# Kernel tuning notes

Measured on AMD Instinct MI355X. Metric: run time of the kernel, lower is better.

The kernel has to match this reference:

```python
import jax, jax.numpy as jnp
import numpy as np

SEQ, BATCH = 256, 8
N_NODES = SEQ * BATCH
VOCAB, D_MODEL, H, D_K, D_FF, N_LAYERS, MAX_POS = 259, 256, 8, 32, 1024, 2, 128


def setup_inputs() -> dict:
    key = jax.random.key(0)
    ks = jax.random.split(key, 16)
    # structured causal edge list per sequence (dst attends to src <= dst, incl. self)
    tri_dst, tri_src = np.tril_indices(SEQ)
    offs = (np.arange(BATCH) * SEQ)[:, None]
    edge_src = jnp.asarray((tri_src[None, :] + offs).ravel(), dtype=jnp.int64)
    edge_dst = jnp.asarray((tri_dst[None, :] + offs).ravel(), dtype=jnp.int64)
    positions = jnp.tile(jnp.arange(SEQ, dtype=jnp.int64), BATCH)
    tokens = jax.random.randint(ks[0], (N_NODES,), 0, VOCAB, dtype=jnp.int64)
    s = 0.02
    p = lambda k, shp: jax.random.normal(k, shp, dtype=jnp.float32) * s
    return {
        "tokens": tokens, "positions": positions,
        "edge_src": edge_src, "edge_dst": edge_dst,
        "coord_emb": p(ks[1], (3, D_MODEL)),
        "pos_emb": p(ks[2], (MAX_POS, D_MODEL)),
        "value_emb": p(ks[3], (VOCAB, D_MODEL)),
        "ln1_scale": jnp.ones((N_LAYERS, D_MODEL)), "ln1_bias": jnp.zeros((N_LAYERS, D_MODEL)),
        "Wqkv": p(ks[4], (N_LAYERS, D_MODEL, 3 * D_MODEL)),
        "Wo": p(ks[5], (N_LAYERS, D_MODEL, D_MODEL)),
        "ln2_scale": jnp.ones((N_LAYERS, D_MODEL)), "ln2_bias": jnp.zeros((N_LAYERS, D_MODEL)),
        "W1": p(ks[6], (N_LAYERS, D_MODEL, D_FF)), "b1": jnp.zeros((N_LAYERS, D_FF)),
        "W2": p(ks[7], (N_LAYERS, D_FF, D_MODEL)), "b2": jnp.zeros((N_LAYERS, D_MODEL)),
        "lnf_scale": jnp.ones((D_MODEL,)), "lnf_bias": jnp.zeros((D_MODEL,)),
        "Wg": p(ks[8], (D_MODEL, VOCAB)), "bg": jnp.zeros((VOCAB,)),
    }


def _ln(x, scale, bias, eps=1e-5):
    mu = jnp.mean(x, axis=-1, keepdims=True)
    var = jnp.var(x, axis=-1, keepdims=True)
    return (x - mu) * jax.lax.rsqrt(var + eps) * scale + bias


def _graph_attention(x, src, dst, Wqkv, Wo, ln_s, ln_b):
    n = x.shape[0]
    xn = _ln(x, ln_s, ln_b)
    qkv = (xn @ Wqkv).reshape(n, 3, H, D_K)
    q, k, v = qkv[:, 0], qkv[:, 1], qkv[:, 2]  # [n, H, D_K] each
    # u_dot_v('k','q','score') per edge, scaled
    score = jnp.einsum("ehd,ehd->eh", k[src], q[dst]) / jnp.sqrt(jnp.float32(D_K))
    # edge_softmax over incoming edges of each dst node
    smax = jax.ops.segment_max(score, dst, num_segments=n)      # [n, H]
    ex = jnp.exp(score - smax[dst])                              # [E, H]
    denom = jax.ops.segment_sum(ex, dst, num_segments=n)        # [n, H]
    alpha = ex / denom[dst]
    # u_mul_e('v','softmax_score') + sum reduce -> z on dst nodes
    z = jax.ops.segment_sum(alpha[:, :, None] * v[src], dst, num_segments=n)  # [n, H, D_K]
    return x + z.reshape(n, D_MODEL) @ Wo


def reference(tokens, positions, edge_src, edge_dst, coord_emb, pos_emb, value_emb,
              ln1_scale, ln1_bias, Wqkv, Wo, ln2_scale, ln2_bias, W1, b1, W2, b2,
              lnf_scale, lnf_bias, Wg, bg):
    x = coord_emb[positions % 3] + pos_emb[positions // 3] + value_emb[tokens]
    for i in range(Wqkv.shape[0]):
        x = _graph_attention(x, edge_src, edge_dst, Wqkv[i], Wo[i], ln1_scale[i], ln1_bias[i])
        h = _ln(x, ln2_scale[i], ln2_bias[i])
        x = x + jax.nn.relu(h @ W1[i] + b1[i]) @ W2[i] + b2[i]
    out = _ln(x, lnf_scale, lnf_bias) @ Wg + bg
    return jax.nn.log_softmax(out, axis=-1)
```

## Files before the change

### kernel.cpp

```cpp
#include <hip/hip_runtime.h>
#include <hip/hip_bf16.h>

typedef __hip_bfloat16 bf16;
typedef unsigned short ushort_t;
typedef unsigned int uint_t;
typedef __attribute__((ext_vector_type(8))) short short8;
typedef __attribute__((ext_vector_type(4))) float floatx4;

#define D_MODEL 256
#define SEQ     256
#define BATCH   8
#define NN      2048
#define NHEAD   8
#define DK      32
#define DFF     1024
#define VOCAB   259
#define NLAYER  2

#define WQKVT_OFF 0
#define WOT_OFF   393216
#define W1T_OFF   524288
#define W2T_OFF   1048576
#define WGT_OFF   1572864
#define WT_TOTAL  1639168
#define LNP_TOTAL 2560
#define BP_TOTAL  2819

template<bool BF>
__device__ __forceinline__ float ldw(const void* p, int i) {
    if (BF) return __bfloat162float(((const bf16*)p)[i]);
    return ((const float*)p)[i];
}
template<bool BF>
__device__ __forceinline__ ushort_t ldb(const void* p, size_t i) {
    if (BF) return ((const ushort_t*)p)[i];
    bf16 h = __float2bfloat16(((const float*)p)[i]);
    ushort_t u; __builtin_memcpy(&u, &h, 2); return u;
}
template<bool I64>
__device__ __forceinline__ int ldi(const void* p, int i) {
    if (I64) return (int)(((const long long*)p)[i]);
    return ((const int*)p)[i];
}
__device__ __forceinline__ ushort_t f2bs(float f) {
    bf16 h = __float2bfloat16(f);
    ushort_t u; __builtin_memcpy(&u, &h, 2); return u;
}
__device__ __forceinline__ float bs2f(uint_t u16) {
    return __uint_as_float(u16 << 16);
}
__device__ __forceinline__ float wred_sum(float v) {
    #pragma unroll
    for (int m = 32; m > 0; m >>= 1) v += __shfl_xor(v, m, 64);
    return v;
}
__device__ __forceinline__ float wred_max(float v) {
    #pragma unroll
    for (int m = 32; m > 0; m >>= 1) v = fmaxf(v, __shfl_xor(v, m, 64));
    return v;
}
__device__ __forceinline__ bool detBF(const void* ln1s) {
    return *(const uint_t*)ln1s == 0x3F803F80u;
}
__device__ __forceinline__ bool detI64(const void* pos) {
    const int* p32 = (const int*)pos;
    return p32[1] == 0 && p32[2] == 1;
}

template<bool BF>
__device__ void ttile(const void* src, size_t srcOff, int K, int N, int tk, int tn,
                      ushort_t* dst, ushort_t (*tile)[68]) {
    int t = threadIdx.x;
    #pragma unroll
    for (int pass = 0; pass < 16; ++pass) {
        int e = pass * 256 + t;
        int kl = e >> 6, nl = e & 63;
        int n = tn * 64 + nl;
        tile[kl][nl] = (n < N) ? ldb<BF>(src, srcOff + (size_t)(tk*64 + kl) * N + n)
                               : (ushort_t)0;
    }
    __syncthreads();
    #pragma unroll
    for (int pass = 0; pass < 16; ++pass) {
        int e = pass * 256 + t;
        int nl = e >> 6, kl = e & 63;
        int n = tn * 64 + nl;
        if (n < N) dst[(size_t)n * K + tk*64 + kl] = tile[kl][nl];
    }
}

template<bool BF, bool I64>
__device__ void embedln16(const void* tok, const void* pos,
        const void* ce, const void* pe, const void* ve,
        const void* ln1s, const void* ln1b, int rowBase,
        float* x, ushort_t* xn) {
    int lane = threadIdx.x & 63, wave = threadIdx.x >> 6;
    #pragma unroll
    for (int i = 0; i < 4; ++i) {
        int n = rowBase + wave * 4 + i;
        int p  = ldi<I64>(pos, n);
        int tk = ldi<I64>(tok, n);
        int c0 = lane * 4;
        float v[4];
        #pragma unroll
        for (int j = 0; j < 4; ++j)
            v[j] = ldw<BF>(ce, (p % 3) * 256 + c0 + j)
                 + ldw<BF>(pe, (p / 3) * 256 + c0 + j)
                 + ldw<BF>(ve, tk * 256 + c0 + j);
        float s  = wred_sum(v[0] + v[1] + v[2] + v[3]);
        float s2 = wred_sum(v[0]*v[0] + v[1]*v[1] + v[2]*v[2] + v[3]*v[3]);
        float mu = s * (1.f/256.f);
        float var = s2 * (1.f/256.f) - mu * mu;
        float rstd = rsqrtf(var + 1e-5f);
        *reinterpret_cast<float4*>(&x[(size_t)n*256 + c0]) =
            make_float4(v[0], v[1], v[2], v[3]);
        ushort4 o;
        o.x = f2bs((v[0]-mu)*rstd*ldw<BF>(ln1s, c0+0) + ldw<BF>(ln1b, c0+0));
        o.y = f2bs((v[1]-mu)*rstd*ldw<BF>(ln1s, c0+1) + ldw<BF>(ln1b, c0+1));
        o.z = f2bs((v[2]-mu)*rstd*ldw<BF>(ln1s, c0+2) + ldw<BF>(ln1b, c0+2));
        o.w = f2bs((v[3]-mu)*rstd*ldw<BF>(ln1s, c0+3) + ldw<BF>(ln1b, c0+3));
        *reinterpret_cast<ushort4*>(&xn[(size_t)n*256 + c0]) = o;
    }
}

template<bool BF, bool I64>
__device__ void prep_body(const void* tok, const void* pos,
        const void* ce, const void* pe, const void* ve,
        const void* Wqkv, const void* Wo, const void* W1, const void* W2, const void* Wg,
        const void* ln1s, const void* ln1b, const void* ln2s, const void* ln2b,
        const void* lnfs, const void* lnfb,
        const void* b1, const void* b2, const void* bg,
        ushort_t* WT, float* lnP, float* bP, float* x, ushort_t* xn,
        ushort_t (*tile)[68]) {
    int blk = blockIdx.x;
    if (blk < 404) {
        const void* src; int K, N, tk, tn; size_t dstOff, srcOff;
        if (blk < 96)       { int L = blk/48, lo = blk%48; src=Wqkv; K=256; N=768;
                              srcOff=(size_t)L*196608; dstOff=WQKVT_OFF+(size_t)L*196608;
                              tk=lo/12; tn=lo%12; }
        else if (blk < 128) { int b2=blk-96, L=b2/16, lo=b2%16; src=Wo; K=256; N=256;
                              srcOff=(size_t)L*65536; dstOff=WOT_OFF+(size_t)L*65536;
                              tk=lo/4; tn=lo%4; }
        else if (blk < 256) { int b2=blk-128, L=b2/64, lo=b2%64; src=W1; K=256; N=1024;
                              srcOff=(size_t)L*262144; dstOff=W1T_OFF+(size_t)L*262144;
                              tk=lo/16; tn=lo%16; }
        else if (blk < 384) { int b2=blk-256, L=b2/64, lo=b2%64; src=W2; K=1024; N=256;
                              srcOff=(size_t)L*262144; dstOff=W2T_OFF+(size_t)L*262144;
                              tk=lo/4; tn=lo%4; }
        else                { int lo=blk-384; src=Wg; K=256; N=259;
                              srcOff=0; dstOff=WGT_OFF; tk=lo/5; tn=lo%5; }
        ttile<BF>(src, srcOff, K, N, tk, tn, WT + dstOff, tile);
    } else if (blk < 426) {
        int gid = (blk - 404) * 256 + threadIdx.x;
        if (gid < LNP_TOTAL) {
            float v;
            if      (gid < 512)  v = ldw<BF>(ln1s, gid);
            else if (gid < 1024) v = ldw<BF>(ln1b, gid - 512);
            else if (gid < 1536) v = ldw<BF>(ln2s, gid - 1024);
            else if (gid < 2048) v = ldw<BF>(ln2b, gid - 1536);
            else if (gid < 2304) v = ldw<BF>(lnfs, gid - 2048);
            else                 v = ldw<BF>(lnfb, gid - 2304);
            lnP[gid] = v;
        } else if (gid < LNP_TOTAL + BP_TOTAL) {
            int g = gid - LNP_TOTAL;
            float v;
            if      (g < 2048) v = ldw<BF>(b1, g);
            else if (g < 2560) v = ldw<BF>(b2, g - 2048);
            else               v = ldw<BF>(bg, g - 2560);
            bP[g] = v;
        }
    } else {
        embedln16<BF, I64>(tok, pos, ce, pe, ve, ln1s, ln1b, (blk - 426) * 16, x, xn);
    }
}

__global__ void __launch_bounds__(256) prep_k(const void* tok, const void* pos,
        const void* ce, const void* pe, const void* ve,
        const void* Wqkv, const void* Wo, const void* W1, const void* W2, const void* Wg,
        const void* ln1s, const void* ln1b, const void* ln2s, const void* ln2b,
        const void* lnfs, const void* lnfb,
        const void* b1, const void* b2, const void* bg,
        ushort_t* WT, float* lnP, float* bP, float* x, ushort_t* xn) {
    __shared__ ushort_t tile[64][68];
    bool BF = detBF(ln1s), I64 = detI64(pos);
    if (BF) { if (I64) prep_body<true,true >(tok,pos,ce,pe,ve,Wqkv,Wo,W1,W2,Wg,ln1s,ln1b,ln2s,ln2b,lnfs,lnfb,b1,b2,bg,WT,lnP,bP,x,xn,tile);
              else     prep_body<true,false>(tok,pos,ce,pe,ve,Wqkv,Wo,W1,W2,Wg,ln1s,ln1b,ln2s,ln2b,lnfs,lnfb,b1,b2,bg,WT,lnP,bP,x,xn,tile); }
    else    { if (I64) prep_body<false,true >(tok,pos,ce,pe,ve,Wqkv,Wo,W1,W2,Wg,ln1s,ln1b,ln2s,ln2b,lnfs,lnfb,b1,b2,bg,WT,lnP,bP,x,xn,tile);
              else     prep_body<false,false>(tok,pos,ce,pe,ve,Wqkv,Wo,W1,W2,Wg,ln1s,ln1b,ln2s,ln2b,lnfs,lnfb,b1,b2,bg,WT,lnP,bP,x,xn,tile); }
}

union AttnSH {
    struct {
        ushort_t Ks[SEQ][40];
        ushort_t Qs[64][40];
    } a;
    ushort_t Ps[64][264];
};
__global__ void __launch_bounds__(256) attn_k(const ushort_t* __restrict__ qkvB,
                                              ushort_t* __restrict__ zB) {
    __shared__ AttnSH u;
    __shared__ ushort_t Vt[32][264];
    int t = threadIdx.x;
    int lane = t & 63, wave = t >> 6;
    int quad = lane >> 4, l16 = lane & 15;
    int tile = blockIdx.x & 3, bh = blockIdx.x >> 2;
    int b = bh >> 3, h = bh & 7;
    int base = b * SEQ;
    int dstBase = tile * 64;
    int tileEnd = (tile + 1) * 64;

    int nV = tileEnd * 4;
    for (int i = t; i < nV; i += 256) {
        int src = i >> 2, g = i & 3;
        const ushort_t* rp = qkvB + (size_t)(base + src) * 768 + h * 32 + g * 8;
        uint4 kv = *reinterpret_cast<const uint4*>(rp + 256);
        *reinterpret_cast<uint4*>(&u.a.Ks[src][g * 8]) = kv;
        uint4 vv = *reinterpret_cast<const uint4*>(rp + 512);
        const ushort_t* vs = (const ushort_t*)&vv;
        #pragma unroll
        for (int j = 0; j < 8; ++j) Vt[g * 8 + j][src] = vs[j];
    }
    {
        int r = t >> 2, g = t & 3;
        uint4 qv = *reinterpret_cast<const uint4*>(
            qkvB + (size_t)(base + dstBase + r) * 768 + h * 32 + g * 8);
        *reinterpret_cast<uint4*>(&u.a.Qs[r][g * 8]) = qv;
    }
    __syncthreads();

    const float scale = 0.17677669529663687f;
    int stLim = tile * 4 + wave;
    int stCnt = stLim + 1;
    short8 qf = *reinterpret_cast<const short8*>(&u.a.Qs[wave * 16 + l16][quad * 8]);
    floatx4 accs[16];
    #pragma unroll
    for (int st = 0; st < 16; ++st) {
        if (st <= stLim) {
            short8 kf = *reinterpret_cast<const short8*>(&u.a.Ks[st * 16 + l16][quad * 8]);
            accs[st] = __builtin_amdgcn_mfma_f32_16x16x32_bf16(qf, kf, (floatx4){0.f,0.f,0.f,0.f}, 0, 0, 0);
        }
    }
    float mrow[4] = {-3e38f, -3e38f, -3e38f, -3e38f};
    #pragma unroll
    for (int st = 0; st < 16; ++st) {
        if (st <= stLim) {
            int srcg = st * 16 + l16;
            #pragma unroll
            for (int r = 0; r < 4; ++r) {
                int dstg = dstBase + wave * 16 + quad * 4 + r;
                float sv = (srcg <= dstg) ? accs[st][r] * scale : -3e38f;
                accs[st][r] = sv;
                mrow[r] = fmaxf(mrow[r], sv);
            }
        }
    }
    #pragma unroll
    for (int mk = 1; mk < 16; mk <<= 1)
        #pragma unroll
        for (int r = 0; r < 4; ++r) mrow[r] = fmaxf(mrow[r], __shfl_xor(mrow[r], mk, 64));
    float lrow[4] = {0.f, 0.f, 0.f, 0.f};
    #pragma unroll
    for (int st = 0; st < 16; ++st) {
        if (st <= stLim) {
            #pragma unroll
            for (int r = 0; r < 4; ++r) {
                float p = __expf(accs[st][r] - mrow[r]);
                accs[st][r] = p;
                lrow[r] += p;
            }
        }
    }
    #pragma unroll
    for (int mk = 1; mk < 16; mk <<= 1)
        #pragma unroll
        for (int r = 0; r < 4; ++r) lrow[r] += __shfl_xor(lrow[r], mk, 64);
    __syncthreads();

    #pragma unroll
    for (int st = 0; st < 16; ++st) {
        if (st <= stLim) {
            #pragma unroll
            for (int r = 0; r < 4; ++r)
                u.Ps[wave * 16 + quad * 4 + r][st * 16 + l16] = f2bs(accs[st][r]);
        }
    }
    if (stCnt & 1) {
        #pragma unroll
        for (int r = 0; r < 4; ++r)
            u.Ps[wave * 16 + quad * 4 + r][stCnt * 16 + l16] = 0;
    }
    __syncthreads();

    int ktCnt = (stCnt + 1) >> 1;
    floatx4 acco[2];
    acco[0] = (floatx4){0.f,0.f,0.f,0.f};
    acco[1] = (floatx4){0.f,0.f,0.f,0.f};
    #pragma unroll
    for (int kt = 0; kt < 8; ++kt) {
        if (kt < ktCnt) {
            short8 pf = *reinterpret_cast<const short8*>(&u.Ps[wave * 16 + l16][kt * 32 + quad * 8]);
            #pragma unroll
            for (int dn = 0; dn < 2; ++dn) {
                short8 vf = *reinterpret_cast<const short8*>(&Vt[dn * 16 + l16][kt * 32 + quad * 8]);
                acco[dn] = __builtin_amdgcn_mfma_f32_16x16x32_bf16(pf, vf, acco[dn], 0, 0, 0);
            }
        }
    }
    #pragma unroll
    for (int dn = 0; dn < 2; ++dn)
        #pragma unroll
        for (int r = 0; r < 4; ++r)
            zB[(size_t)(base + dstBase + wave * 16 + quad * 4 + r) * 256
               + h * 32 + dn * 16 + l16] = f2bs(acco[dn][r] / lrow[r]);
}

__global__ void __launch_bounds__(256) gemm_k(const ushort_t* __restrict__ A, int K,
        const ushort_t* __restrict__ BT, const float* __restrict__ bias,
        ushort_t* __restrict__ C, int ldc, int relu) {
    int t = threadIdx.x;
    int lane = t & 63, wave = t >> 6;
    int quad = lane >> 4, l16 = lane & 15;
    int wm = (wave >> 1) * 32, wn = (wave & 1) * 32;
    int rowBase = blockIdx.x * 64, colBase = blockIdx.y * 64;
    floatx4 acc[2][2];
    #pragma unroll
    for (int a = 0; a < 2; ++a)
        #pragma unroll
        for (int b = 0; b < 2; ++b) acc[a][b] = (floatx4){0.f,0.f,0.f,0.f};
    const ushort_t* a0 = A + (size_t)(rowBase + wm + l16) * K + quad * 8;
    const ushort_t* a1 = a0 + (size_t)16 * K;
    const ushort_t* b0 = BT + (size_t)(colBase + wn + l16) * K + quad * 8;
    const ushort_t* b1 = b0 + (size_t)16 * K;
    #pragma unroll 8
    for (int k0 = 0; k0 < K; k0 += 32) {
        short8 af0 = *reinterpret_cast<const short8*>(a0 + k0);
        short8 af1 = *reinterpret_cast<const short8*>(a1 + k0);
        short8 bf0 = *reinterpret_cast<const short8*>(b0 + k0);
        short8 bf1 = *reinterpret_cast<const short8*>(b1 + k0);
        acc[0][0] = __builtin_amdgcn_mfma_f32_16x16x32_bf16(af0, bf0, acc[0][0], 0,0,0);
        acc[0][1] = __builtin_amdgcn_mfma_f32_16x16x32_bf16(af0, bf1, acc[0][1], 0,0,0);
        acc[1][0] = __builtin_amdgcn_mfma_f32_16x16x32_bf16(af1, bf0, acc[1][0], 0,0,0);
        acc[1][1] = __builtin_amdgcn_mfma_f32_16x16x32_bf16(af1, bf1, acc[1][1], 0,0,0);
    }
    #pragma unroll
    for (int nt = 0; nt < 2; ++nt) {
        int col = colBase + wn + nt*16 + l16;
        float bb = bias ? bias[col] : 0.f;
        #pragma unroll
        for (int mt = 0; mt < 2; ++mt)
            #pragma unroll
            for (int r = 0; r < 4; ++r) {
                int row = rowBase + wm + mt*16 + quad*4 + r;
                float v = acc[mt][nt][r] + bb;
                if (relu) v = fmaxf(v, 0.f);
                C[(size_t)row * ldc + col] = f2bs(v);
            }
    }
}

__global__ void __launch_bounds__(256) gemmresln_k(const ushort_t* __restrict__ A, int K,
        const ushort_t* __restrict__ BT, const float* __restrict__ bias,
        float* __restrict__ x, const float* __restrict__ ls, const float* __restrict__ lb,
        ushort_t* __restrict__ xnG,
        const void* __restrict__ ln1sRaw, const ushort_t* __restrict__ WgT,
        const float* __restrict__ bgP, void* __restrict__ outp, int doLogits) {
    __shared__ float sparts[4][16][256];
    __shared__ ushort_t xnS[16][264];
    float (*Lg)[273] = reinterpret_cast<float (*)[273]>(&sparts[1][0][0]);
    int t = threadIdx.x;
    int lane = t & 63, wave = t >> 6;
    int quad = lane >> 4, l16 = lane & 15;
    int rowBase = blockIdx.x * 16;
    int Kq = K >> 2;
    int wk0 = wave * Kq;

    {
        floatx4 acc[16];
        #pragma unroll
        for (int nt = 0; nt < 16; ++nt) acc[nt] = (floatx4){0.f,0.f,0.f,0.f};
        const ushort_t* a0 = A + (size_t)(rowBase + l16) * K + wk0 + quad * 8;
        for (int k0 = 0; k0 < Kq; k0 += 32) {
            short8 af = *reinterpret_cast<const short8*>(a0 + k0);
            #pragma unroll
            for (int nt = 0; nt < 16; ++nt) {
                short8 bv = *reinterpret_cast<const short8*>(
                    BT + (size_t)(nt*16 + l16) * K + wk0 + k0 + quad * 8);
                acc[nt] = __builtin_amdgcn_mfma_f32_16x16x32_bf16(af, bv, acc[nt], 0,0,0);
            }
        }
        #pragma unroll
        for (int nt = 0; nt < 16; ++nt)
            #pragma unroll
            for (int r = 0; r < 4; ++r)
                sparts[wave][quad*4 + r][nt*16 + l16] = acc[nt][r];
    }
    __syncthreads();
    {
        float* flat0 = &sparts[0][0][0];
        #pragma unroll
        for (int i = 0; i < 16; ++i) {
            int idx = i * 256 + t;
            int row = idx >> 8, col = idx & 255;
            float v = flat0[idx] + (&sparts[1][0][0])[idx]
                    + (&sparts[2][0][0])[idx] + (&sparts[3][0][0])[idx];
            if (bias) v += bias[col];
            v += x[(size_t)(rowBase + row) * 256 + col];
            x[(size_t)(rowBase + row) * 256 + col] = v;
            flat0[idx] = v;
        }
    }
    __syncthreads();
    #pragma unroll
    for (int i = 0; i < 4; ++i) {
        int row = wave*4 + i;
        int c0 = lane * 4;
        float4 vv = *reinterpret_cast<const float4*>(&sparts[0][row][c0]);
        float s  = wred_sum(vv.x + vv.y + vv.z + vv.w);
        float s2 = wred_sum(vv.x*vv.x + vv.y*vv.y + vv.z*vv.z + vv.w*vv.w);
        float mu = s * (1.f/256.f);
        float var = s2 * (1.f/256.f) - mu*mu;
        float rstd = rsqrtf(var + 1e-5f);
        ushort4 o;
        o.x = f2bs((vv.x-mu)*rstd*ls[c0+0] + lb[c0+0]);
        o.y = f2bs((vv.y-mu)*rstd*ls[c0+1] + lb[c0+1]);
        o.z = f2bs((vv.z-mu)*rstd*ls[c0+2] + lb[c0+2]);
        o.w = f2bs((vv.w-mu)*rstd*ls[c0+3] + lb[c0+3]);
        *reinterpret_cast<ushort4*>(&xnG[(size_t)(rowBase+row)*256 + c0]) = o;
        if (doLogits) *reinterpret_cast<ushort4*>(&xnS[row][c0]) = o;
    }
    if (!doLogits) return;
    __syncthreads();
    int cb = wave * 64;
    const ushort_t* a0 = &xnS[l16][quad * 8];
    {
        floatx4 acc[4];
        #pragma unroll
        for (int nt = 0; nt < 4; ++nt) acc[nt] = (floatx4){0.f,0.f,0.f,0.f};
        #pragma unroll
        for (int kc = 0; kc < 8; ++kc) {
            short8 af = *reinterpret_cast<const short8*>(a0 + kc * 32);
            #pragma unroll
            for (int nt = 0; nt < 4; ++nt) {
                short8 bv = *reinterpret_cast<const short8*>(
                    WgT + (size_t)(cb + nt*16 + l16) * 256 + kc*32 + quad*8);
                acc[nt] = __builtin_amdgcn_mfma_f32_16x16x32_bf16(af, bv, acc[nt], 0,0,0);
            }
        }
        __syncthreads();
        #pragma unroll
        for (int nt = 0; nt < 4; ++nt) {
            int col = cb + nt*16 + l16;
            float bb = bgP[col];
            #pragma unroll
            for (int r = 0; r < 4; ++r)
                Lg[quad*4 + r][col] = acc[nt][r] + bb;
        }
    }
    if (wave == 0) {
        floatx4 acc = (floatx4){0.f,0.f,0.f,0.f};
        int n = 256 + l16;
        int nc = (n < VOCAB) ? n : 0;
        const ushort_t* b0 = WgT + (size_t)nc * 256 + quad * 8;
        #pragma unroll
        for (int kc = 0; kc < 8; ++kc) {
            short8 af = *reinterpret_cast<const short8*>(a0 + kc * 32);
            short8 bv = *reinterpret_cast<const short8*>(b0 + kc * 32);
            acc = __builtin_amdgcn_mfma_f32_16x16x32_bf16(af, bv, acc, 0,0,0);
        }
        #pragma unroll
        for (int r = 0; r < 4; ++r)
            Lg[quad*4 + r][256 + l16] = (n < VOCAB) ? (acc[r] + bgP[n]) : -1e30f;
    }
    __syncthreads();
    int outBF = detBF(ln1sRaw) ? 1 : 0;
    #pragma unroll
    for (int i = 0; i < 4; ++i) {
        int row = wave*4 + i;
        float v0 = Lg[row][lane],     v1 = Lg[row][lane+64];
        float v2 = Lg[row][lane+128], v3 = Lg[row][lane+192];
        float v4 = (lane < 16) ? Lg[row][256+lane] : -1e30f;
        float m = wred_max(fmaxf(fmaxf(fmaxf(v0,v1), fmaxf(v2,v3)), v4));
        float se = __expf(v0-m) + __expf(v1-m) + __expf(v2-m) + __expf(v3-m)
                 + ((lane < 16) ? __expf(v4-m) : 0.f);
        se = wred_sum(se);
        float lse = m + logf(se);
        size_t nbase = (size_t)(rowBase + row) * VOCAB;
        if (outBF) {
            ushort_t* o = (ushort_t*)outp + nbase;
            o[lane]     = f2bs(v0 - lse);
            o[lane+64]  = f2bs(v1 - lse);
            o[lane+128] = f2bs(v2 - lse);
            o[lane+192] = f2bs(v3 - lse);
            if (lane < 3) o[256+lane] = f2bs(v4 - lse);
        } else {
            float* o = (float*)outp + nbase;
            o[lane]     = v0 - lse;
            o[lane+64]  = v1 - lse;
            o[lane+128] = v2 - lse;
            o[lane+192] = v3 - lse;
            if (lane < 3) o[256+lane] = v4 - lse;
        }
    }
}

extern "C" void kernel_launch(void* const* d_in, const int* in_sizes, int n_in,
                              void* d_out, int out_size, void* d_ws, size_t ws_size,
                              hipStream_t stream) {
    const void* tok  = d_in[0];
    const void* pos  = d_in[1];
    const void* ce   = d_in[4];
    const void* pe   = d_in[5];
    const void* ve   = d_in[6];
    const void* ln1s = d_in[7];
    const void* ln1b = d_in[8];
    const void* Wqkv = d_in[9];
    const void* Wo   = d_in[10];
    const void* ln2s = d_in[11];
    const void* ln2b = d_in[12];
    const void* W1   = d_in[13];
    const void* b1   = d_in[14];
    const void* W2   = d_in[15];
    const void* b2   = d_in[16];
    const void* lnfs = d_in[17];
    const void* lnfb = d_in[18];
    const void* Wg   = d_in[19];
    const void* bg   = d_in[20];

    char* base = (char*)d_ws;
    float*    lnP  = (float*)base;
    float*    bP   = (float*)(base + 10240);
    float*    x    = (float*)(base + 22528);
    ushort_t* xn   = (ushort_t*)(base + 2119680);
    ushort_t* zB   = (ushort_t*)(base + 3168256);
    ushort_t* ffB  = (ushort_t*)(base + 4216832);
    ushort_t* WT   = (ushort_t*)(base + 8411136);
    ushort_t* qkvB = (ushort_t*)(base + 11689472);

    prep_k<<<554, 256, 0, stream>>>(tok, pos, ce, pe, ve,
        Wqkv, Wo, W1, W2, Wg, ln1s, ln1b, ln2s, ln2b, lnfs, lnfb,
        b1, b2, bg, WT, lnP, bP, x, xn);
    for (int L = 0; L < NLAYER; ++L) {
        gemm_k<<<dim3(32, 12), 256, 0, stream>>>(xn, 256,
            WT + WQKVT_OFF + (size_t)L * 768 * 256, nullptr, qkvB, 768, 0);
        attn_k<<<256, 256, 0, stream>>>(qkvB, zB);
        gemmresln_k<<<128, 256, 0, stream>>>(zB, 256,
            WT + WOT_OFF + (size_t)L * 256 * 256, nullptr,
            x, lnP + 1024 + L * 256, lnP + 1536 + L * 256, xn,
            ln1s, WT + WGT_OFF, bP + 2560, d_out, 0);
        gemm_k<<<dim3(32, 16), 256, 0, stream>>>(xn, 256,
            WT + W1T_OFF + (size_t)L * 1024 * 256, bP + L * 1024, ffB, 1024, 1);
        const float* lsN = (L == 0) ? (lnP + 256)       : (lnP + 2048);
        const float* lbN = (L == 0) ? (lnP + 512 + 256) : (lnP + 2304);
        gemmresln_k<<<128, 256, 0, stream>>>(ffB, 1024,
            WT + W2T_OFF + (size_t)L * 256 * 1024, bP + 2048 + L * 256,
            x, lsN, lbN, xn,
            ln1s, WT + WGT_OFF, bP + 2560, d_out, (L == NLAYER - 1) ? 1 : 0);
    }
}
```

Measured before the change: 239.3 us.

## Fuse attention output, FFN, layernorms and next-layer QKV into one tail kernel

Replaces the per-layer chain of Wo GEMM+residual+LN, W1 GEMM, and W2 GEMM+residual+LN with a single tail kernel per layer. Each 16-row block keeps the FFN hidden activations in shared memory and also computes the next layer's QKV projection, or the final logits. This removes several launches and the global round-trips of the FFN intermediate and normalized activations. The cost is only 128 blocks doing all the heavy GEMM work, each re-reading full weight matrices from global memory, so lower parallelism and more weight traffic per block.

After: 228.6 us. 1.05x faster.

```diff
diff --git a/kernel.cpp b/kernel.cpp
--- a/kernel.cpp
+++ b/kernel.cpp
@@ -26,6 +26,10 @@
 #define LNP_TOTAL 2560
 #define BP_TOTAL  2819
 
+__device__ __forceinline__ ushort_t f2bs(float f) {
+    bf16 h = __float2bfloat16(f);
+    ushort_t u; __builtin_memcpy(&u, &h, 2); return u;
+}
 template<bool BF>
 __device__ __forceinline__ float ldw(const void* p, int i) {
     if (BF) return __bfloat162float(((const bf16*)p)[i]);
@@ -34,20 +38,12 @@
 template<bool BF>
 __device__ __forceinline__ ushort_t ldb(const void* p, size_t i) {
     if (BF) return ((const ushort_t*)p)[i];
-    bf16 h = __float2bfloat16(((const float*)p)[i]);
-    ushort_t u; __builtin_memcpy(&u, &h, 2); return u;
+    return f2bs(((const float*)p)[i]);
 }
 template<bool I64>
 __device__ __forceinline__ int ldi(const void* p, int i) {
     if (I64) return (int)(((const long long*)p)[i]);
     return ((const int*)p)[i];
-}
-__device__ __forceinline__ ushort_t f2bs(float f) {
-    bf16 h = __float2bfloat16(f);
-    ushort_t u; __builtin_memcpy(&u, &h, 2); return u;
-}
-__device__ __forceinline__ float bs2f(uint_t u16) {
-    return __uint_as_float(u16 << 16);
 }
 __device__ __forceinline__ float wred_sum(float v) {
     #pragma unroll
@@ -358,63 +354,19 @@
     }
 }
 
-__global__ void __launch_bounds__(256) gemmresln_k(const ushort_t* __restrict__ A, int K,
-        const ushort_t* __restrict__ BT, const float* __restrict__ bias,
-        float* __restrict__ x, const float* __restrict__ ls, const float* __restrict__ lb,
-        ushort_t* __restrict__ xnG,
-        const void* __restrict__ ln1sRaw, const ushort_t* __restrict__ WgT,
-        const float* __restrict__ bgP, void* __restrict__ outp, int doLogits) {
-    __shared__ float sparts[4][16][256];
-    __shared__ ushort_t xnS[16][264];
-    float (*Lg)[273] = reinterpret_cast<float (*)[273]>(&sparts[1][0][0]);
-    int t = threadIdx.x;
-    int lane = t & 63, wave = t >> 6;
-    int quad = lane >> 4, l16 = lane & 15;
-    int rowBase = blockIdx.x * 16;
-    int Kq = K >> 2;
-    int wk0 = wave * Kq;
-
-    {
-        floatx4 acc[16];
-        #pragma unroll
-        for (int nt = 0; nt < 16; ++nt) acc[nt] = (floatx4){0.f,0.f,0.f,0.f};
-        const ushort_t* a0 = A + (size_t)(rowBase + l16) * K + wk0 + quad * 8;
-        for (int k0 = 0; k0 < Kq; k0 += 32) {
-            short8 af = *reinterpret_cast<const short8*>(a0 + k0);
-            #pragma unroll
-            for (int nt = 0; nt < 16; ++nt) {
-                short8 bv = *reinterpret_cast<const short8*>(
-                    BT + (size_t)(nt*16 + l16) * K + wk0 + k0 + quad * 8);
-                acc[nt] = __builtin_amdgcn_mfma_f32_16x16x32_bf16(af, bv, acc[nt], 0,0,0);
-            }
-        }
-        #pragma unroll
-        for (int nt = 0; nt < 16; ++nt)
-            #pragma unroll
-            for (int r = 0; r < 4; ++r)
-                sparts[wave][quad*4 + r][nt*16 + l16] = acc[nt][r];
-    }
-    __syncthreads();
-    {
-        float* flat0 = &sparts[0][0][0];
-        #pragma unroll
-        for (int i = 0; i < 16; ++i) {
-            int idx = i * 256 + t;
-            int row = idx >> 8, col = idx & 255;
-            float v = flat0[idx] + (&sparts[1][0][0])[idx]
-                    + (&sparts[2][0][0])[idx] + (&sparts[3][0][0])[idx];
-            if (bias) v += bias[col];
-            v += x[(size_t)(rowBase + row) * 256 + col];
-            x[(size_t)(rowBase + row) * 256 + col] = v;
-            flat0[idx] = v;
-        }
-    }
-    __syncthreads();
+union TailHU {
+    ushort_t hmid[16][1032];
+    float    Lg[16][273];
+};
+
+__device__ __forceinline__ void ln16_store(const float (*xrow)[256],
+        const float* __restrict__ ls, const float* __restrict__ lb,
+        ushort_t (*xnA)[264]) {
+    int lane = threadIdx.x & 63, wave = threadIdx.x >> 6;
     #pragma unroll
     for (int i = 0; i < 4; ++i) {
-        int row = wave*4 + i;
-        int c0 = lane * 4;
-        float4 vv = *reinterpret_cast<const float4*>(&sparts[0][row][c0]);
+        int row = wave*4 + i, c0 = lane * 4;
+        float4 vv = *reinterpret_cast<const float4*>(&xrow[row][c0]);
         float s  = wred_sum(vv.x + vv.y + vv.z + vv.w);
         float s2 = wred_sum(vv.x*vv.x + vv.y*vv.y + vv.z*vv.z + vv.w*vv.w);
         float mu = s * (1.f/256.f);
@@ -425,80 +377,211 @@
         o.y = f2bs((vv.y-mu)*rstd*ls[c0+1] + lb[c0+1]);
         o.z = f2bs((vv.z-mu)*rstd*ls[c0+2] + lb[c0+2]);
         o.w = f2bs((vv.w-mu)*rstd*ls[c0+3] + lb[c0+3]);
-        *reinterpret_cast<ushort4*>(&xnG[(size_t)(rowBase+row)*256 + c0]) = o;
-        if (doLogits) *reinterpret_cast<ushort4*>(&xnS[row][c0]) = o;
-    }
-    if (!doLogits) return;
-    __syncthreads();
+        *reinterpret_cast<ushort4*>(&xnA[row][c0]) = o;
+    }
+}
+
+__global__ void __launch_bounds__(256) tail_k(
+        const ushort_t* __restrict__ zB,
+        const ushort_t* __restrict__ WoT,
+        float* __restrict__ x,
+        const float* __restrict__ ls2, const float* __restrict__ lb2,
+        const ushort_t* __restrict__ W1T, const float* __restrict__ b1P,
+        const ushort_t* __restrict__ W2T, const float* __restrict__ b2P,
+        const float* __restrict__ lsN, const float* __restrict__ lbN,
+        const ushort_t* __restrict__ WqkvTn, ushort_t* __restrict__ qkvB,
+        const ushort_t* __restrict__ WgT, const float* __restrict__ bgP,
+        const void* __restrict__ ln1sRaw, void* __restrict__ outp, int doLogits) {
+    __shared__ ushort_t xnA[16][264];
+    __shared__ float    xrow[16][256];
+    __shared__ TailHU   hu;
+    int t = threadIdx.x, lane = t & 63, wave = t >> 6;
+    int quad = lane >> 4, l16 = lane & 15;
+    int rowBase = blockIdx.x * 16;
     int cb = wave * 64;
-    const ushort_t* a0 = &xnS[l16][quad * 8];
+    float vpre[4][4];
+
     {
         floatx4 acc[4];
         #pragma unroll
         for (int nt = 0; nt < 4; ++nt) acc[nt] = (floatx4){0.f,0.f,0.f,0.f};
-        #pragma unroll
-        for (int kc = 0; kc < 8; ++kc) {
-            short8 af = *reinterpret_cast<const short8*>(a0 + kc * 32);
+        const ushort_t* a0 = zB + (size_t)(rowBase + l16) * 256 + quad * 8;
+        #pragma unroll
+        for (int k0 = 0; k0 < 256; k0 += 32) {
+            short8 af = *reinterpret_cast<const short8*>(a0 + k0);
             #pragma unroll
             for (int nt = 0; nt < 4; ++nt) {
                 short8 bv = *reinterpret_cast<const short8*>(
-                    WgT + (size_t)(cb + nt*16 + l16) * 256 + kc*32 + quad*8);
+                    WoT + (size_t)(cb + nt*16 + l16) * 256 + k0 + quad * 8);
                 acc[nt] = __builtin_amdgcn_mfma_f32_16x16x32_bf16(af, bv, acc[nt], 0,0,0);
             }
         }
-        __syncthreads();
         #pragma unroll
         for (int nt = 0; nt < 4; ++nt) {
             int col = cb + nt*16 + l16;
-            float bb = bgP[col];
+            #pragma unroll
+            for (int r = 0; r < 4; ++r) {
+                int row = quad*4 + r;
+                float v = acc[nt][r] + x[(size_t)(rowBase + row) * 256 + col];
+                vpre[nt][r] = v;
+                xrow[row][col] = v;
+            }
+        }
+    }
+    __syncthreads();
+    ln16_store(xrow, ls2, lb2, xnA);
+    __syncthreads();
+
+    {
+        floatx4 acc[16];
+        #pragma unroll
+        for (int nt = 0; nt < 16; ++nt) acc[nt] = (floatx4){0.f,0.f,0.f,0.f};
+        const ushort_t* a0 = &xnA[l16][quad * 8];
+        #pragma unroll
+        for (int k0 = 0; k0 < 256; k0 += 32) {
+            short8 af = *reinterpret_cast<const short8*>(a0 + k0);
+            #pragma unroll
+            for (int nt = 0; nt < 16; ++nt) {
+                short8 bv = *reinterpret_cast<const short8*>(
+                    W1T + (size_t)(wave*256 + nt*16 + l16) * 256 + k0 + quad * 8);
+                acc[nt] = __builtin_amdgcn_mfma_f32_16x16x32_bf16(af, bv, acc[nt], 0,0,0);
+            }
+        }
+        #pragma unroll
+        for (int nt = 0; nt < 16; ++nt) {
+            int col = wave*256 + nt*16 + l16;
+            float bb = b1P[col];
             #pragma unroll
             for (int r = 0; r < 4; ++r)
-                Lg[quad*4 + r][col] = acc[nt][r] + bb;
-        }
-    }
-    if (wave == 0) {
-        floatx4 acc = (floatx4){0.f,0.f,0.f,0.f};
-        int n = 256 + l16;
-        int nc = (n < VOCAB) ? n : 0;
-        const ushort_t* b0 = WgT + (size_t)nc * 256 + quad * 8;
-        #pragma unroll
-        for (int kc = 0; kc < 8; ++kc) {
-            short8 af = *reinterpret_cast<const short8*>(a0 + kc * 32);
-            short8 bv = *reinterpret_cast<const short8*>(b0 + kc * 32);
-            acc = __builtin_amdgcn_mfma_f32_16x16x32_bf16(af, bv, acc, 0,0,0);
-        }
-        #pragma unroll
-        for (int r = 0; r < 4; ++r)
-            Lg[quad*4 + r][256 + l16] = (n < VOCAB) ? (acc[r] + bgP[n]) : -1e30f;
-    }
-    __syncthreads();
-    int outBF = detBF(ln1sRaw) ? 1 : 0;
-    #pragma unroll
-    for (int i = 0; i < 4; ++i) {
-        int row = wave*4 + i;
-        float v0 = Lg[row][lane],     v1 = Lg[row][lane+64];
-        float v2 = Lg[row][lane+128], v3 = Lg[row][lane+192];
-        float v4 = (lane < 16) ? Lg[row][256+lane] : -1e30f;
-        float m = wred_max(fmaxf(fmaxf(fmaxf(v0,v1), fmaxf(v2,v3)), v4));
-        float se = __expf(v0-m) + __expf(v1-m) + __expf(v2-m) + __expf(v3-m)
-                 + ((lane < 16) ? __expf(v4-m) : 0.f);
-        se = wred_sum(se);
-        float lse = m + logf(se);
-        size_t nbase = (size_t)(rowBase + row) * VOCAB;
-        if (outBF) {
-            ushort_t* o = (ushort_t*)outp + nbase;
-            o[lane]     = f2bs(v0 - lse);
-            o[lane+64]  = f2bs(v1 - lse);
-            o[lane+128] = f2bs(v2 - lse);
-            o[lane+192] = f2bs(v3 - lse);
-            if (lane < 3) o[256+lane] = f2bs(v4 - lse);
-        } else {
-            float* o = (float*)outp + nbase;
-            o[lane]     = v0 - lse;
-            o[lane+64]  = v1 - lse;
-            o[lane+128] = v2 - lse;
-            o[lane+192] = v3 - lse;
-            if (lane < 3) o[256+lane] = v4 - lse;
+                hu.hmid[quad*4 + r][col] = f2bs(fmaxf(acc[nt][r] + bb, 0.f));
+        }
+    }
+    __syncthreads();
+
+    {
+        floatx4 acc[4];
+        #pragma unroll
+        for (int nt = 0; nt < 4; ++nt) acc[nt] = (floatx4){0.f,0.f,0.f,0.f};
+        #pragma unroll 8
+        for (int k0 = 0; k0 < 1024; k0 += 32) {
+            short8 af = *reinterpret_cast<const short8*>(&hu.hmid[l16][k0 + quad * 8]);
+            #pragma unroll
+            for (int nt = 0; nt < 4; ++nt) {
+                short8 bv = *reinterpret_cast<const short8*>(
+                    W2T + (size_t)(cb + nt*16 + l16) * 1024 + k0 + quad * 8);
+                acc[nt] = __builtin_amdgcn_mfma_f32_16x16x32_bf16(af, bv, acc[nt], 0,0,0);
+            }
+        }
+        #pragma unroll
+        for (int nt = 0; nt < 4; ++nt) {
+            int col = cb + nt*16 + l16;
+            float bb = b2P[col];
+            #pragma unroll
+            for (int r = 0; r < 4; ++r) {
+                int row = quad*4 + r;
+                float v = acc[nt][r] + bb + vpre[nt][r];
+                x[(size_t)(rowBase + row) * 256 + col] = v;
+                xrow[row][col] = v;
+            }
+        }
+    }
+    __syncthreads();
+    ln16_store(xrow, lsN, lbN, xnA);
+    __syncthreads();
+
+    if (WqkvTn) {
+        floatx4 acc[12];
+        #pragma unroll
+        for (int nt = 0; nt < 12; ++nt) acc[nt] = (floatx4){0.f,0.f,0.f,0.f};
+        const ushort_t* a0 = &xnA[l16][quad * 8];
+        #pragma unroll
+        for (int k0 = 0; k0 < 256; k0 += 32) {
+            short8 af = *reinterpret_cast<const short8*>(a0 + k0);
+            #pragma unroll
+            for (int nt = 0; nt < 12; ++nt) {
+                short8 bv = *reinterpret_cast<const short8*>(
+                    WqkvTn + (size_t)(wave*192 + nt*16 + l16) * 256 + k0 + quad * 8);
+                acc[nt] = __builtin_amdgcn_mfma_f32_16x16x32_bf16(af, bv, acc[nt], 0,0,0);
+            }
+        }
+        #pragma unroll
+        for (int nt = 0; nt < 12; ++nt) {
+            int col = wave*192 + nt*16 + l16;
+            #pragma unroll
+            for (int r = 0; r < 4; ++r)
+                qkvB[(size_t)(rowBase + quad*4 + r) * 768 + col] = f2bs(acc[nt][r]);
+        }
+    }
+
+    if (doLogits) {
+        const ushort_t* a0 = &xnA[l16][quad * 8];
+        {
+            floatx4 acc[4];
+            #pragma unroll
+            for (int nt = 0; nt < 4; ++nt) acc[nt] = (floatx4){0.f,0.f,0.f,0.f};
+            #pragma unroll
+            for (int kc = 0; kc < 8; ++kc) {
+                short8 af = *reinterpret_cast<const short8*>(a0 + kc * 32);
+                #pragma unroll
+                for (int nt = 0; nt < 4; ++nt) {
+                    short8 bv = *reinterpret_cast<const short8*>(
+                        WgT + (size_t)(cb + nt*16 + l16) * 256 + kc*32 + quad*8);
+                    acc[nt] = __builtin_amdgcn_mfma_f32_16x16x32_bf16(af, bv, acc[nt], 0,0,0);
+                }
+            }
+            #pragma unroll
+            for (int nt = 0; nt < 4; ++nt) {
+                int col = cb + nt*16 + l16;
+                float bb = bgP[col];
+                #pragma unroll
+                for (int r = 0; r < 4; ++r)
+                    hu.Lg[quad*4 + r][col] = acc[nt][r] + bb;
+            }
+        }
+        if (wave == 0) {
+            floatx4 acc = (floatx4){0.f,0.f,0.f,0.f};
+            int n = 256 + l16;
+            int nc = (n < VOCAB) ? n : 0;
+            const ushort_t* b0 = WgT + (size_t)nc * 256 + quad * 8;
+            #pragma unroll
+            for (int kc = 0; kc < 8; ++kc) {
+                short8 af = *reinterpret_cast<const short8*>(a0 + kc * 32);
+                short8 bv = *reinterpret_cast<const short8*>(b0 + kc * 32);
+                acc = __builtin_amdgcn_mfma_f32_16x16x32_bf16(af, bv, acc, 0,0,0);
+            }
+            #pragma unroll
+            for (int r = 0; r < 4; ++r)
+                hu.Lg[quad*4 + r][256 + l16] = (n < VOCAB) ? (acc[r] + bgP[n]) : -1e30f;
+        }
+        __syncthreads();
+        int outBF = detBF(ln1sRaw) ? 1 : 0;
+        #pragma unroll
+        for (int i = 0; i < 4; ++i) {
+            int row = wave*4 + i;
+            float v0 = hu.Lg[row][lane],     v1 = hu.Lg[row][lane+64];
+            float v2 = hu.Lg[row][lane+128], v3 = hu.Lg[row][lane+192];
+            float v4 = (lane < 16) ? hu.Lg[row][256+lane] : -1e30f;
+            float m = wred_max(fmaxf(fmaxf(fmaxf(v0,v1), fmaxf(v2,v3)), v4));
+            float se = __expf(v0-m) + __expf(v1-m) + __expf(v2-m) + __expf(v3-m)
+                     + ((lane < 16) ? __expf(v4-m) : 0.f);
+            se = wred_sum(se);
+            float lse = m + logf(se);
+            size_t nbase = (size_t)(rowBase + row) * VOCAB;
+            if (outBF) {
+                ushort_t* o = (ushort_t*)outp + nbase;
+                o[lane]     = f2bs(v0 - lse);
+                o[lane+64]  = f2bs(v1 - lse);
+                o[lane+128] = f2bs(v2 - lse);
+                o[lane+192] = f2bs(v3 - lse);
+                if (lane < 3) o[256+lane] = f2bs(v4 - lse);
+            } else {
+                float* o = (float*)outp + nbase;
+                o[lane]     = v0 - lse;
+                o[lane+64]  = v1 - lse;
+                o[lane+128] = v2 - lse;
+                o[lane+192] = v3 - lse;
+                if (lane < 3) o[256+lane] = v4 - lse;
+            }
         }
     }
 }
@@ -532,28 +615,31 @@
     float*    x    = (float*)(base + 22528);
     ushort_t* xn   = (ushort_t*)(base + 2119680);
     ushort_t* zB   = (ushort_t*)(base + 3168256);
-    ushort_t* ffB  = (ushort_t*)(base + 4216832);
     ushort_t* WT   = (ushort_t*)(base + 8411136);
     ushort_t* qkvB = (ushort_t*)(base + 11689472);
 
     prep_k<<<554, 256, 0, stream>>>(tok, pos, ce, pe, ve,
         Wqkv, Wo, W1, W2, Wg, ln1s, ln1b, ln2s, ln2b, lnfs, lnfb,
         b1, b2, bg, WT, lnP, bP, x, xn);
-    for (int L = 0; L < NLAYER; ++L) {
-        gemm_k<<<dim3(32, 12), 256, 0, stream>>>(xn, 256,
-            WT + WQKVT_OFF + (size_t)L * 768 * 256, nullptr, qkvB, 768, 0);
-        attn_k<<<256, 256, 0, stream>>>(qkvB, zB);
-        gemmresln_k<<<128, 256, 0, stream>>>(zB, 256,
-            WT + WOT_OFF + (size_t)L * 256 * 256, nullptr,
-            x, lnP + 1024 + L * 256, lnP + 1536 + L * 256, xn,
-            ln1s, WT + WGT_OFF, bP + 2560, d_out, 0);
-        gemm_k<<<dim3(32, 16), 256, 0, stream>>>(xn, 256,
-            WT + W1T_OFF + (size_t)L * 1024 * 256, bP + L * 1024, ffB, 1024, 1);
-        const float* lsN = (L == 0) ? (lnP + 256)       : (lnP + 2048);
-        const float* lbN = (L == 0) ? (lnP + 512 + 256) : (lnP + 2304);
-        gemmresln_k<<<128, 256, 0, stream>>>(ffB, 1024,
-            WT + W2T_OFF + (size_t)L * 256 * 1024, bP + 2048 + L * 256,
-            x, lsN, lbN, xn,
-            ln1s, WT + WGT_OFF, bP + 2560, d_out, (L == NLAYER - 1) ? 1 : 0);
-    }
-}
+
+    gemm_k<<<dim3(32, 12), 256, 0, stream>>>(xn, 256,
+        WT + WQKVT_OFF, nullptr, qkvB, 768, 0);
+
+    attn_k<<<256, 256, 0, stream>>>(qkvB, zB);
+
+    tail_k<<<128, 256, 0, stream>>>(zB,
+        WT + WOT_OFF, x, lnP + 1024, lnP + 1536,
+        WT + W1T_OFF, bP, WT + W2T_OFF, bP + 2048,
+        lnP + 256, lnP + 768,
+        WT + WQKVT_OFF + 196608, qkvB,
+        WT + WGT_OFF, bP + 2560, ln1s, d_out, 0);
+
+    attn_k<<<256, 256, 0, stream>>>(qkvB, zB);
+
+    tail_k<<<128, 256, 0, stream>>>(zB,
+        WT + WOT_OFF + 65536, x, lnP + 1024 + 256, lnP + 1536 + 256,
+        WT + W1T_OFF + 262144, bP + 1024, WT + W2T_OFF + 262144, bP + 2048 + 256,
+        lnP + 2048, lnP + 2304,
+        nullptr, qkvB,
+        WT + WGT_OFF, bP + 2560, ln1s, d_out, 1);
+}
```
